# Performance work log

Measured on AMD Instinct MI355X. Metric: run time of the kernel, lower is better.

## Reference

```python
import jax, jax.numpy as jnp
import numpy as np
from jax import lax

C = 768
CA = C // 4  # adapter_channels = 192
L = 197      # 1 CLS + 14*14 patches
T_FRAMES = 16
B = 16
N = B * T_FRAMES


def quick_gelu(x):
    return x * jax.nn.sigmoid(1.702 * x)


def setup_inputs() -> dict:
    key = jax.random.key(0)
    ks = jax.random.split(key, 16)
    s = 0.02
    return {
        "x": jax.random.normal(ks[0], (L, N, C), dtype=jnp.float32),
        "T": T_FRAMES,
        # main path (fc1 -> depthwise conv1d over T -> fc2)
        "fc1_w": jax.random.normal(ks[1], (C, CA), jnp.float32) * s,
        "fc1_b": jnp.zeros((CA,), jnp.float32),
        "conv_w": jax.random.normal(ks[2], (CA, 1, 3), jnp.float32) * s,  # (O, I/g, K)
        "conv_b": jnp.zeros((CA,), jnp.float32),
        "fc2_w": jax.random.normal(ks[3], (CA, C), jnp.float32) * s,
        "fc2_b": jnp.zeros((C,), jnp.float32),
        # offset adapter (fc1 -> depthwise conv3d (1,3,3) -> fc2)
        "off_fc1_w": jax.random.normal(ks[4], (C, CA), jnp.float32) * s,
        "off_fc1_b": jnp.zeros((CA,), jnp.float32),
        "off_conv_w": jax.random.normal(ks[5], (CA, 1, 1, 3, 3), jnp.float32) * s,  # (O, I/g, D, H, W)
        "off_conv_b": jnp.zeros((CA,), jnp.float32),
        "off_fc2_w": jax.random.normal(ks[6], (CA, C), jnp.float32) * s,
        "off_fc2_b": jnp.zeros((C,), jnp.float32),
        # mlp branch (c_in -> QuickGELU -> c_out)
        "mlp_in_w": jax.random.normal(ks[7], (C, CA), jnp.float32) * s,
        "mlp_in_b": jnp.zeros((CA,), jnp.float32),
        "mlp_out_w": jax.random.normal(ks[8], (CA, C), jnp.float32) * s,
        "mlp_out_b": jnp.zeros((C,), jnp.float32),
    }


def _offset_adapter(x, T, fc1_w, fc1_b, conv_w, conv_b, fc2_w, fc2_b):
    Lx, Nx, Cx = x.shape
    Bx = Nx // T
    HW = Lx - 1
    H = int(round(HW ** 0.5))
    Ca = fc1_w.shape[1]
    xp = jnp.transpose(x, (1, 0, 2))            # (N, L, C)
    xs = xp[:, 1:, :].reshape(Bx, T, HW, Cx)    # (B, T, HW, C)
    # former frame: index [0, 0, 1, ..., T-2]
    x_former = jnp.concatenate([xs[:, :1], xs[:, :-1]], axis=1)
    off = xs - x_former
    off = off @ fc1_w + fc1_b                   # (B, T, HW, Ca)
    off = off.reshape(Bx, T, H, H, Ca).transpose(0, 4, 1, 2, 3)  # (B, Ca, T, H, W)
    off = lax.conv_general_dilated(
        off, conv_w, window_strides=(1, 1, 1),
        padding=[(0, 0), (1, 1), (1, 1)],
        dimension_numbers=("NCDHW", "OIDHW", "NCDHW"),
        feature_group_count=Ca,
    ) + conv_b[None, :, None, None, None]
    off = off.transpose(0, 2, 3, 4, 1).reshape(Nx, HW, Ca)
    off = off @ fc2_w + fc2_b                   # (N, L-1, C)
    return jnp.transpose(off, (1, 0, 2))        # (L-1, N, C)


def reference(x, T, fc1_w, fc1_b, conv_w, conv_b, fc2_w, fc2_b,
              off_fc1_w, off_fc1_b, off_conv_w, off_conv_b, off_fc2_w, off_fc2_b,
              mlp_in_w, mlp_in_b, mlp_out_w, mlp_out_b):
    Lx, Nx, Cx = x.shape
    Bx = Nx // T
    Ca = fc1_w.shape[1]

    offset = _offset_adapter(x, T, off_fc1_w, off_fc1_b, off_conv_w, off_conv_b,
                             off_fc2_w, off_fc2_b)  # (L-1, N, C)

    # mlp identity branch
    x_id = quick_gelu(x @ mlp_in_w + mlp_in_b) @ mlp_out_w + mlp_out_b  # (L, N, C)

    # main branch: fc1 -> depthwise conv1d along T -> fc2
    h = x @ fc1_w + fc1_b                                   # (L, N, Ca)
    h = jnp.transpose(h, (1, 0, 2)).reshape(Bx, T, Lx, Ca)  # (B, T, L, Ca)
    h = h.transpose(0, 2, 3, 1).reshape(Bx * Lx, Ca, T)     # (B*L, Ca, T)
    h = lax.conv_general_dilated(
        h, conv_w, window_strides=(1,), padding=[(1, 1)],
        dimension_numbers=("NCH", "OIH", "NCH"),
        feature_group_count=Ca,
    ) + conv_b[None, :, None]
    h = h.transpose(0, 2, 1).reshape(Bx, Lx, T, Ca)
    h = h.transpose(0, 2, 1, 3).reshape(Nx, Lx, Ca)
    h = jnp.transpose(h, (1, 0, 2))                         # (L, N, Ca)
    h = h @ fc2_w + fc2_b                                   # (L, N, C)

    x_id = x_id.at[1:].add(offset)
    return h + x_id
```

## Files before the change

kernel.cpp:

```cpp
#include <hip/hip_runtime.h>

#define L_DIM 197
#define N_DIM 256
#define C_DIM 768
#define CA_DIM 192
#define M_DIM (L_DIM * N_DIM)

typedef short s16x8 __attribute__((ext_vector_type(8)));
typedef float f32x4 __attribute__((ext_vector_type(4)));

__device__ __forceinline__ unsigned short f2bf(float f) {
  unsigned x = __builtin_bit_cast(unsigned, f);
  x = (x + 0x7fffu + ((x >> 16) & 1u)) >> 16;
  return (unsigned short)x;
}
__device__ __forceinline__ float bflo(unsigned u) { return __builtin_bit_cast(float, u << 16); }
__device__ __forceinline__ float bfhi(unsigned u) { return __builtin_bit_cast(float, u & 0xffff0000u); }

__device__ __forceinline__ void unp8(uint4 v, float* f) {
  f[0] = bflo(v.x); f[1] = bfhi(v.x); f[2] = bflo(v.y); f[3] = bfhi(v.y);
  f[4] = bflo(v.z); f[5] = bfhi(v.z); f[6] = bflo(v.w); f[7] = bfhi(v.w);
}

__device__ __forceinline__ void mfma16(f32x4& acc, s16x8 a, s16x8 b) {
  asm("v_mfma_f32_16x16x32_bf16 %0, %1, %2, %0" : "+v"(acc) : "v"(a), "v"(b));
}

typedef const void __attribute__((address_space(1)))* gp_t;
typedef void __attribute__((address_space(3)))* lp_t;
__device__ __forceinline__ void gl16(const void* g, void* l) {
  __builtin_amdgcn_global_load_lds((gp_t)g, (lp_t)l, 16, 0, 0);
}

#define WAITVM(n) asm volatile("s_waitcnt vmcnt(" #n ")" ::: "memory")

__device__ __forceinline__ int swz(int pid, int nwg) {
  const int q = nwg >> 3, r = nwg & 7, x = pid & 7, s = pid >> 3;
  return (x < r ? x * (q + 1) : r * (q + 1) + (x - r) * q) + s;
}

__global__ __launch_bounds__(256) void prep_k(
    const float* __restrict__ fc1_w, const float* __restrict__ mlp_in_w,
    const float* __restrict__ off_fc1_w, const float* __restrict__ fc2_w,
    const float* __restrict__ mlp_out_w, const float* __restrict__ off_fc2_w,
    unsigned short* __restrict__ wa, unsigned short* __restrict__ wc) {
  __shared__ float t[32][33];
  const int b = blockIdx.x;
  const int job = b / 144, tt = b - job * 144;
  const float* in = job == 0 ? fc1_w : job == 1 ? mlp_in_w : job == 2 ? off_fc1_w
                  : job == 3 ? fc2_w : job == 4 ? mlp_out_w : off_fc2_w;
  const int Cc = job < 3 ? 192 : 768;
  const int tc = Cc >> 5;
  const int tr0 = (tt / tc) << 5, tc0 = (tt - (tt / tc) * tc) << 5;
  const int lr = threadIdx.x >> 5, lc = threadIdx.x & 31;
#pragma unroll
  for (int p = 0; p < 4; p++)
    t[p * 8 + lr][lc] = in[(tr0 + p * 8 + lr) * Cc + tc0 + lc];
  __syncthreads();
#pragma unroll
  for (int p = 0; p < 4; p++) {
    const int orow = tc0 + p * 8 + lr;
    const int ocol = tr0 + lc;
    const unsigned short v = f2bf(t[lc][p * 8 + lr]);
    if (job < 3) wa[(job * 192 + orow) * 768 + ocol] = v;
    else         wc[orow * 576 + (job - 3) * 192 + ocol] = v;
  }
}

__global__ __launch_bounds__(256) void xcvt_k(const float* __restrict__ x,
                                              unsigned short* __restrict__ xb) {
  const int total8 = M_DIM * C_DIM / 8;
  const int step = gridDim.x * 256;
  for (int i = blockIdx.x * 256 + threadIdx.x; i < total8; i += step) {
    const float4 a = *(const float4*)(x + (size_t)i * 8);
    const float4 b = *(const float4*)(x + (size_t)i * 8 + 4);
    s16x8 v;
    v[0] = (short)f2bf(a.x); v[1] = (short)f2bf(a.y);
    v[2] = (short)f2bf(a.z); v[3] = (short)f2bf(a.w);
    v[4] = (short)f2bf(b.x); v[5] = (short)f2bf(b.y);
    v[6] = (short)f2bf(b.z); v[7] = (short)f2bf(b.w);
    *(s16x8*)(xb + (size_t)i * 8) = v;
  }
}

__global__ __launch_bounds__(256, 2) void gemm_a_k(
    const unsigned short* __restrict__ xb, const unsigned short* __restrict__ wa,
    const float* __restrict__ fc1_b, const float* __restrict__ mlp_in_b,
    const float* __restrict__ cw, const float* __restrict__ cb,
    const float* __restrict__ off_b1, unsigned short* __restrict__ hcat) {
  __shared__ unsigned short As[2][64 * 32];
  __shared__ unsigned short Bs[2][576 * 32];
  const int tid = threadIdx.x, lane = tid & 63, w = tid >> 6;
  const int m0 = blockIdx.x * 64;

  const int sr = tid >> 2, sc = (tid & 3) * 8;
  const unsigned short* gA = xb + (size_t)(m0 + sr) * C_DIM + sc;
  const unsigned short* gB = wa + (size_t)sr * C_DIM + sc;

  auto stage = [&](int kt, int b) {
    gl16(gA + kt * 32, &As[b][sr * 32 + sc]);
    const unsigned short* pb = gB + kt * 32;
#pragma unroll
    for (int j = 0; j < 9; j++)
      gl16(pb + (size_t)j * 64 * C_DIM, &Bs[b][(j * 64 + sr) * 32 + sc]);
  };

  f32x4 acc[4][9];
#pragma unroll
  for (int i = 0; i < 4; i++)
#pragma unroll
    for (int j = 0; j < 9; j++) acc[i][j] = (f32x4){0.f, 0.f, 0.f, 0.f};

  const int fr = lane & 15, fq = lane >> 4;
  const int wn = w * 144;

  stage(0, 0);
  __syncthreads();
#pragma unroll 2
  for (int kt = 0; kt < 24; ++kt) {
    const int b = kt & 1;
    if (kt + 1 < 24) stage(kt + 1, b ^ 1);
    s16x8 af[4];
#pragma unroll
    for (int mi = 0; mi < 4; mi++)
      af[mi] = *(const s16x8*)&As[b][(mi * 16 + fr) * 32 + fq * 8];
#pragma unroll
    for (int ni = 0; ni < 9; ni++) {
      const s16x8 bf_ = *(const s16x8*)&Bs[b][(wn + ni * 16 + fr) * 32 + fq * 8];
#pragma unroll
      for (int mi = 0; mi < 4; mi++) mfma16(acc[mi][ni], af[mi], bf_);
    }
    __syncthreads();
  }

  const bool zrow = (m0 < 256);
#pragma unroll
  for (int ni = 0; ni < 9; ni++) {
    const int cb_ = wn + ni * 16;
    const int path = cb_ / 192;
    const int ca = cb_ % 192 + fr;
    if (path == 0) {
      const float bv = fc1_b[ca];
      const float w0 = cw[ca * 3], w1 = cw[ca * 3 + 1], w2 = cw[ca * 3 + 2];
      const float cbv = cb[ca];
#pragma unroll
      for (int mi = 0; mi < 4; mi++) {
        const float v0 = acc[mi][ni][0] + bv, v1 = acc[mi][ni][1] + bv;
        const float v2 = acc[mi][ni][2] + bv, v3 = acc[mi][ni][3] + bv;
        const float pv3 = __shfl_up(v3, 16);
        const float nv0 = __shfl_down(v0, 16);
        const float p0 = fq > 0 ? pv3 : 0.f;
        const float n3 = fq < 3 ? nv0 : 0.f;
        const int mb = m0 + mi * 16 + fq * 4;
        hcat[(size_t)(mb + 0) * 576 + ca] = f2bf(w0 * p0 + w1 * v0 + w2 * v1 + cbv);
        hcat[(size_t)(mb + 1) * 576 + ca] = f2bf(w0 * v0 + w1 * v1 + w2 * v2 + cbv);
        hcat[(size_t)(mb + 2) * 576 + ca] = f2bf(w0 * v1 + w1 * v2 + w2 * v3 + cbv);
        hcat[(size_t)(mb + 3) * 576 + ca] = f2bf(w0 * v2 + w1 * v3 + w2 * n3 + cbv);
      }
    } else if (path == 1) {
      const float bv = mlp_in_b[ca];
#pragma unroll
      for (int mi = 0; mi < 4; mi++)
#pragma unroll
        for (int r = 0; r < 4; r++) {
          const int m = m0 + mi * 16 + fq * 4 + r;
          float v = acc[mi][ni][r] + bv;
          v = v / (1.f + __expf(-1.702f * v));
          hcat[(size_t)m * 576 + 192 + ca] = f2bf(v);
        }
    } else {
      const float bv = off_b1[ca];
#pragma unroll
      for (int mi = 0; mi < 4; mi++) {
        const float v0 = acc[mi][ni][0], v1 = acc[mi][ni][1];
        const float v2 = acc[mi][ni][2], v3 = acc[mi][ni][3];
        const float pv3 = __shfl_up(v3, 16);
        const int mb = m0 + mi * 16 + fq * 4;
        const float o0 = (fq == 0) ? bv : (v0 - pv3 + bv);
        if (zrow) {
          hcat[(size_t)(mb + 0) * 576 + 384 + ca] = 0;
          hcat[(size_t)(mb + 1) * 576 + 384 + ca] = 0;
          hcat[(size_t)(mb + 2) * 576 + 384 + ca] = 0;
          hcat[(size_t)(mb + 3) * 576 + 384 + ca] = 0;
        } else {
          hcat[(size_t)(mb + 0) * 576 + 384 + ca] = f2bf(o0);
          hcat[(size_t)(mb + 1) * 576 + 384 + ca] = f2bf(v1 - v0 + bv);
          hcat[(size_t)(mb + 2) * 576 + 384 + ca] = f2bf(v2 - v1 + bv);
          hcat[(size_t)(mb + 3) * 576 + 384 + ca] = f2bf(v3 - v2 + bv);
        }
      }
    }
  }
}

__global__ __launch_bounds__(256) void conv3d_k(
    const float* __restrict__ w3, const float* __restrict__ b2,
    unsigned short* __restrict__ hcat) {
  __shared__ float ds[196 * 48];
  __shared__ float w3s[9 * 48];
  __shared__ float b2s[48];
  const int blk = blockIdx.x;
  const int n = blk >> 2, q = blk & 3;
  const int ch0 = q * 48;
  const int tid = threadIdx.x;

  for (int j = tid; j < 432; j += 256) {
    const int c = j / 9, tap = j % 9;
    w3s[tap * 48 + c] = w3[(ch0 + c) * 9 + tap];
  }
  if (tid < 48) b2s[tid] = b2[ch0 + tid];

  for (int j = tid; j < 196 * 6; j += 256) {
    const int hw = j / 6, ck = j % 6;
    float dv[8];
    unp8(*(const uint4*)(hcat + ((size_t)(1 + hw) * 256 + n) * 576 + 384 + ch0 + ck * 8), dv);
#pragma unroll
    for (int e = 0; e < 8; e++) ds[hw * 48 + ck * 8 + e] = dv[e];
  }
  __syncthreads();

  for (int j = tid; j < 196 * 6; j += 256) {
    const int hw = j / 6, ck = j % 6;
    const int i = hw / 14, j0 = hw - i * 14;
    float acc[8];
#pragma unroll
    for (int e = 0; e < 8; e++) acc[e] = b2s[ck * 8 + e];
#pragma unroll
    for (int di = 0; di < 3; di++) {
      const int ii = i + di - 1;
      if (ii < 0 || ii >= 14) continue;
#pragma unroll
      for (int dj = 0; dj < 3; dj++) {
        const int jc = j0 + dj - 1;
        if (jc < 0 || jc >= 14) continue;
        const float* dp = &ds[(ii * 14 + jc) * 48 + ck * 8];
        const float* wp = &w3s[(di * 3 + dj) * 48 + ck * 8];
#pragma unroll
        for (int e = 0; e < 8; e++) acc[e] += wp[e] * dp[e];
      }
    }
    unsigned o[4];
#pragma unroll
    for (int e = 0; e < 8; e += 2)
      o[e / 2] = (unsigned)f2bf(acc[e]) | ((unsigned)f2bf(acc[e + 1]) << 16);
    uint4 ov; ov.x = o[0]; ov.y = o[1]; ov.z = o[2]; ov.w = o[3];
    *(uint4*)(hcat + ((size_t)(1 + hw) * 256 + n) * 576 + 384 + ch0 + ck * 8) = ov;
  }
}

__global__ __launch_bounds__(256, 1) void gemm_c_k(
    const unsigned short* __restrict__ hcat, const unsigned short* __restrict__ wc,
    const float* __restrict__ fc2_b, const float* __restrict__ mlp_out_b,
    const float* __restrict__ off_fc2_b, float* __restrict__ out) {
  __shared__ unsigned short As[3][128 * 32];
  __shared__ unsigned short Bs[3][256 * 32];
  const int tid = threadIdx.x, lane = tid & 63, w = tid >> 6;
  const int lid = swz(blockIdx.x, 3 * 394);
  const int by = lid / 3, bx = lid - by * 3;
  const int m0 = by * 128, n0 = bx * 256;

  const int sr = tid >> 2, sc = (tid & 3) * 8;
  const unsigned short* gA = hcat + (size_t)(m0 + sr) * 576 + sc;
  const unsigned short* gB = wc + (size_t)(n0 + sr) * 576 + sc;
  auto stage = [&](int kt, int b) {
#pragma unroll
    for (int j = 0; j < 2; j++)
      gl16(gA + kt * 32 + j * 64 * 576, &As[b][(sr + j * 64) * 32 + sc]);
#pragma unroll
    for (int j = 0; j < 4; j++)
      gl16(gB + kt * 32 + j * 64 * 576, &Bs[b][(sr + j * 64) * 32 + sc]);
  };

  f32x4 acc[4][8];
#pragma unroll
  for (int i = 0; i < 4; i++)
#pragma unroll
    for (int j = 0; j < 8; j++) acc[i][j] = (f32x4){0.f, 0.f, 0.f, 0.f};

  const int fr = lane & 15, fq = lane >> 4;
  const int wm = (w >> 1) * 64, wn = (w & 1) * 128;

  stage(0, 0);
#pragma unroll 3
  for (int kt = 0; kt < 18; ++kt) {
    const int b = kt % 3;
    if (kt + 1 < 18) { stage(kt + 1, (kt + 1) % 3); WAITVM(6); }
    else             { WAITVM(0); }
    __builtin_amdgcn_s_barrier();
    asm volatile("" ::: "memory");
    s16x8 af[4], bfv[8];
#pragma unroll
    for (int mi = 0; mi < 4; mi++)
      af[mi] = *(const s16x8*)&As[b][(wm + mi * 16 + fr) * 32 + fq * 8];
#pragma unroll
    for (int ni = 0; ni < 8; ni++)
      bfv[ni] = *(const s16x8*)&Bs[b][(wn + ni * 16 + fr) * 32 + fq * 8];
#pragma unroll
    for (int mi = 0; mi < 4; mi++)
#pragma unroll
      for (int ni = 0; ni < 8; ni++) mfma16(acc[mi][ni], af[mi], bfv[ni]);
  }

  float bv[8];
#pragma unroll
  for (int ni = 0; ni < 8; ni++) {
    const int c = n0 + wn + ni * 16 + fr;
    bv[ni] = fc2_b[c] + mlp_out_b[c] + (by >= 2 ? off_fc2_b[c] : 0.f);
  }
#pragma unroll
  for (int mi = 0; mi < 4; mi++)
#pragma unroll
    for (int r = 0; r < 4; r++) {
      const int m = m0 + wm + mi * 16 + fq * 4 + r;
      float* op = out + (size_t)m * C_DIM + n0 + wn;
#pragma unroll
      for (int ni = 0; ni < 8; ni++) op[ni * 16 + fr] = acc[mi][ni][r] + bv[ni];
    }
}

extern "C" void kernel_launch(void* const* d_in, const int* in_sizes, int n_in,
                              void* d_out, int out_size, void* d_ws, size_t ws_size,
                              hipStream_t stream) {
  const float* x          = (const float*)d_in[0];
  const float* fc1_w      = (const float*)d_in[2];
  const float* fc1_b      = (const float*)d_in[3];
  const float* conv_w     = (const float*)d_in[4];
  const float* conv_b     = (const float*)d_in[5];
  const float* fc2_w      = (const float*)d_in[6];
  const float* fc2_b      = (const float*)d_in[7];
  const float* off_fc1_w  = (const float*)d_in[8];
  const float* off_fc1_b  = (const float*)d_in[9];
  const float* off_conv_w = (const float*)d_in[10];
  const float* off_conv_b = (const float*)d_in[11];
  const float* off_fc2_w  = (const float*)d_in[12];
  const float* off_fc2_b  = (const float*)d_in[13];
  const float* mlp_in_w   = (const float*)d_in[14];
  const float* mlp_in_b   = (const float*)d_in[15];
  const float* mlp_out_w  = (const float*)d_in[16];
  const float* mlp_out_b  = (const float*)d_in[17];
  float* out = (float*)d_out;

  char* ws = (char*)d_ws;
  unsigned short* xb   = (unsigned short*)(ws);
  unsigned short* hcat = (unsigned short*)(ws + (size_t)M_DIM * C_DIM * 2);
  unsigned short* wa   = (unsigned short*)(ws + (size_t)M_DIM * C_DIM * 2
                                              + (size_t)M_DIM * 576 * 2);
  unsigned short* wc   = wa + (size_t)576 * 768;

  prep_k<<<864, 256, 0, stream>>>(fc1_w, mlp_in_w, off_fc1_w, fc2_w, mlp_out_w,
                                  off_fc2_w, wa, wc);
  xcvt_k<<<2048, 256, 0, stream>>>(x, xb);
  gemm_a_k<<<788, 256, 0, stream>>>(xb, wa, fc1_b, mlp_in_b, conv_w, conv_b,
                                    off_fc1_b, hcat);
  conv3d_k<<<1024, 256, 0, stream>>>(off_conv_w, off_conv_b, hcat);
  gemm_c_k<<<1182, 256, 0, stream>>>(hcat, wc, fc2_b, mlp_out_b, off_fc2_b, out);
}
```

Baseline: 228.8 us.

## Retile first GEMM to 128x288 with triple-buffered loads and fuse prep kernels

The first GEMM now uses 128-row by 288-column tiles, with two blocks per row band instead of one 64x576 block. Each wave covers a 64x144 sub-tile, and blocks are ordered by a swizzled mapping so weight tiles see better L2 reuse. The shared-memory pipeline goes from two to three buffers, using manual vmcnt waits and a single barrier per k-step instead of two __syncthreads. The weight transpose and x-to-bf16 conversion kernels are merged into one launch to save a kernel launch. The hand-written vmcnt counts depend on how many loads each wave issues, so any miscount risks a race.

New measurement: 209.8 us. 8.3% less time.

```diff
diff --git a/kernel.cpp b/kernel.cpp
--- a/kernel.cpp
+++ b/kernel.cpp
@@ -39,47 +39,48 @@
   return (x < r ? x * (q + 1) : r * (q + 1) + (x - r) * q) + s;
 }
 
-__global__ __launch_bounds__(256) void prep_k(
+__global__ __launch_bounds__(256) void prep_xcvt_k(
     const float* __restrict__ fc1_w, const float* __restrict__ mlp_in_w,
     const float* __restrict__ off_fc1_w, const float* __restrict__ fc2_w,
     const float* __restrict__ mlp_out_w, const float* __restrict__ off_fc2_w,
-    unsigned short* __restrict__ wa, unsigned short* __restrict__ wc) {
+    const float* __restrict__ x,
+    unsigned short* __restrict__ wa, unsigned short* __restrict__ wc,
+    unsigned short* __restrict__ xb) {
   __shared__ float t[32][33];
   const int b = blockIdx.x;
-  const int job = b / 144, tt = b - job * 144;
-  const float* in = job == 0 ? fc1_w : job == 1 ? mlp_in_w : job == 2 ? off_fc1_w
-                  : job == 3 ? fc2_w : job == 4 ? mlp_out_w : off_fc2_w;
-  const int Cc = job < 3 ? 192 : 768;
-  const int tc = Cc >> 5;
-  const int tr0 = (tt / tc) << 5, tc0 = (tt - (tt / tc) * tc) << 5;
-  const int lr = threadIdx.x >> 5, lc = threadIdx.x & 31;
-#pragma unroll
-  for (int p = 0; p < 4; p++)
-    t[p * 8 + lr][lc] = in[(tr0 + p * 8 + lr) * Cc + tc0 + lc];
-  __syncthreads();
-#pragma unroll
-  for (int p = 0; p < 4; p++) {
-    const int orow = tc0 + p * 8 + lr;
-    const int ocol = tr0 + lc;
-    const unsigned short v = f2bf(t[lc][p * 8 + lr]);
-    if (job < 3) wa[(job * 192 + orow) * 768 + ocol] = v;
-    else         wc[orow * 576 + (job - 3) * 192 + ocol] = v;
-  }
-}
-
-__global__ __launch_bounds__(256) void xcvt_k(const float* __restrict__ x,
-                                              unsigned short* __restrict__ xb) {
-  const int total8 = M_DIM * C_DIM / 8;
-  const int step = gridDim.x * 256;
-  for (int i = blockIdx.x * 256 + threadIdx.x; i < total8; i += step) {
-    const float4 a = *(const float4*)(x + (size_t)i * 8);
-    const float4 b = *(const float4*)(x + (size_t)i * 8 + 4);
-    s16x8 v;
-    v[0] = (short)f2bf(a.x); v[1] = (short)f2bf(a.y);
-    v[2] = (short)f2bf(a.z); v[3] = (short)f2bf(a.w);
-    v[4] = (short)f2bf(b.x); v[5] = (short)f2bf(b.y);
-    v[6] = (short)f2bf(b.z); v[7] = (short)f2bf(b.w);
-    *(s16x8*)(xb + (size_t)i * 8) = v;
+  if (b < 864) {
+    const int job = b / 144, tt = b - job * 144;
+    const float* in = job == 0 ? fc1_w : job == 1 ? mlp_in_w : job == 2 ? off_fc1_w
+                    : job == 3 ? fc2_w : job == 4 ? mlp_out_w : off_fc2_w;
+    const int Cc = job < 3 ? 192 : 768;
+    const int tc = Cc >> 5;
+    const int tr0 = (tt / tc) << 5, tc0 = (tt - (tt / tc) * tc) << 5;
+    const int lr = threadIdx.x >> 5, lc = threadIdx.x & 31;
+#pragma unroll
+    for (int p = 0; p < 4; p++)
+      t[p * 8 + lr][lc] = in[(tr0 + p * 8 + lr) * Cc + tc0 + lc];
+    __syncthreads();
+#pragma unroll
+    for (int p = 0; p < 4; p++) {
+      const int orow = tc0 + p * 8 + lr;
+      const int ocol = tr0 + lc;
+      const unsigned short v = f2bf(t[lc][p * 8 + lr]);
+      if (job < 3) wa[(job * 192 + orow) * 768 + ocol] = v;
+      else         wc[orow * 576 + (job - 3) * 192 + ocol] = v;
+    }
+  } else {
+    const int total8 = M_DIM * C_DIM / 8;
+    const int step = 2048 * 256;
+    for (int i = (b - 864) * 256 + threadIdx.x; i < total8; i += step) {
+      const float4 a = *(const float4*)(x + (size_t)i * 8);
+      const float4 c = *(const float4*)(x + (size_t)i * 8 + 4);
+      s16x8 v;
+      v[0] = (short)f2bf(a.x); v[1] = (short)f2bf(a.y);
+      v[2] = (short)f2bf(a.z); v[3] = (short)f2bf(a.w);
+      v[4] = (short)f2bf(c.x); v[5] = (short)f2bf(c.y);
+      v[6] = (short)f2bf(c.z); v[7] = (short)f2bf(c.w);
+      *(s16x8*)(xb + (size_t)i * 8) = v;
+    }
   }
 }
 
@@ -88,21 +89,27 @@
     const float* __restrict__ fc1_b, const float* __restrict__ mlp_in_b,
     const float* __restrict__ cw, const float* __restrict__ cb,
     const float* __restrict__ off_b1, unsigned short* __restrict__ hcat) {
-  __shared__ unsigned short As[2][64 * 32];
-  __shared__ unsigned short Bs[2][576 * 32];
+  __shared__ unsigned short As[3][128 * 32];
+  __shared__ unsigned short Bs[3][288 * 32];
   const int tid = threadIdx.x, lane = tid & 63, w = tid >> 6;
-  const int m0 = blockIdx.x * 64;
+  const int lid = swz(blockIdx.x, 2 * 394);
+  const int by = lid >> 1, bx = lid & 1;
+  const int m0 = by * 128, n0 = bx * 288;
 
   const int sr = tid >> 2, sc = (tid & 3) * 8;
   const unsigned short* gA = xb + (size_t)(m0 + sr) * C_DIM + sc;
-  const unsigned short* gB = wa + (size_t)sr * C_DIM + sc;
+  const unsigned short* gB = wa + (size_t)(n0 + sr) * C_DIM + sc;
 
   auto stage = [&](int kt, int b) {
-    gl16(gA + kt * 32, &As[b][sr * 32 + sc]);
+    const unsigned short* pa = gA + kt * 32;
+    gl16(pa,              &As[b][sr * 32 + sc]);
+    gl16(pa + 64 * C_DIM, &As[b][(64 + sr) * 32 + sc]);
     const unsigned short* pb = gB + kt * 32;
 #pragma unroll
-    for (int j = 0; j < 9; j++)
+    for (int j = 0; j < 4; j++)
       gl16(pb + (size_t)j * 64 * C_DIM, &Bs[b][(j * 64 + sr) * 32 + sc]);
+    if (tid < 128)
+      gl16(pb + (size_t)256 * C_DIM, &Bs[b][(256 + sr) * 32 + sc]);
   };
 
   f32x4 acc[4][9];
@@ -112,33 +119,38 @@
     for (int j = 0; j < 9; j++) acc[i][j] = (f32x4){0.f, 0.f, 0.f, 0.f};
 
   const int fr = lane & 15, fq = lane >> 4;
-  const int wn = w * 144;
+  const int wm = (w >> 1) * 64, wn = (w & 1) * 144;
 
   stage(0, 0);
-  __syncthreads();
-#pragma unroll 2
+#pragma unroll 3
   for (int kt = 0; kt < 24; ++kt) {
-    const int b = kt & 1;
-    if (kt + 1 < 24) stage(kt + 1, b ^ 1);
+    const int b = kt % 3;
+    if (kt + 1 < 24) {
+      stage(kt + 1, (kt + 1) % 3);
+      if (w < 2) { WAITVM(7); } else { WAITVM(6); }
+    } else {
+      WAITVM(0);
+    }
+    __builtin_amdgcn_s_barrier();
+    asm volatile("" ::: "memory");
     s16x8 af[4];
 #pragma unroll
     for (int mi = 0; mi < 4; mi++)
-      af[mi] = *(const s16x8*)&As[b][(mi * 16 + fr) * 32 + fq * 8];
+      af[mi] = *(const s16x8*)&As[b][(wm + mi * 16 + fr) * 32 + fq * 8];
 #pragma unroll
     for (int ni = 0; ni < 9; ni++) {
       const s16x8 bf_ = *(const s16x8*)&Bs[b][(wn + ni * 16 + fr) * 32 + fq * 8];
 #pragma unroll
       for (int mi = 0; mi < 4; mi++) mfma16(acc[mi][ni], af[mi], bf_);
     }
-    __syncthreads();
-  }
-
-  const bool zrow = (m0 < 256);
+  }
+
+  const bool zrow = (by < 2);
 #pragma unroll
   for (int ni = 0; ni < 9; ni++) {
-    const int cb_ = wn + ni * 16;
+    const int cb_ = n0 + wn + ni * 16;
     const int path = cb_ / 192;
-    const int ca = cb_ % 192 + fr;
+    const int ca = cb_ - path * 192 + fr;
     if (path == 0) {
       const float bv = fc1_b[ca];
       const float w0 = cw[ca * 3], w1 = cw[ca * 3 + 1], w2 = cw[ca * 3 + 2];
@@ -151,7 +163,7 @@
         const float nv0 = __shfl_down(v0, 16);
         const float p0 = fq > 0 ? pv3 : 0.f;
         const float n3 = fq < 3 ? nv0 : 0.f;
-        const int mb = m0 + mi * 16 + fq * 4;
+        const int mb = m0 + wm + mi * 16 + fq * 4;
         hcat[(size_t)(mb + 0) * 576 + ca] = f2bf(w0 * p0 + w1 * v0 + w2 * v1 + cbv);
         hcat[(size_t)(mb + 1) * 576 + ca] = f2bf(w0 * v0 + w1 * v1 + w2 * v2 + cbv);
         hcat[(size_t)(mb + 2) * 576 + ca] = f2bf(w0 * v1 + w1 * v2 + w2 * v3 + cbv);
@@ -163,7 +175,7 @@
       for (int mi = 0; mi < 4; mi++)
 #pragma unroll
         for (int r = 0; r < 4; r++) {
-          const int m = m0 + mi * 16 + fq * 4 + r;
+          const int m = m0 + wm + mi * 16 + fq * 4 + r;
           float v = acc[mi][ni][r] + bv;
           v = v / (1.f + __expf(-1.702f * v));
           hcat[(size_t)m * 576 + 192 + ca] = f2bf(v);
@@ -175,7 +187,7 @@
         const float v0 = acc[mi][ni][0], v1 = acc[mi][ni][1];
         const float v2 = acc[mi][ni][2], v3 = acc[mi][ni][3];
         const float pv3 = __shfl_up(v3, 16);
-        const int mb = m0 + mi * 16 + fq * 4;
+        const int mb = m0 + wm + mi * 16 + fq * 4;
         const float o0 = (fq == 0) ? bv : (v0 - pv3 + bv);
         if (zrow) {
           hcat[(size_t)(mb + 0) * 576 + 384 + ca] = 0;
@@ -347,9 +359,8 @@
                                               + (size_t)M_DIM * 576 * 2);
   unsigned short* wc   = wa + (size_t)576 * 768;
 
-  prep_k<<<864, 256, 0, stream>>>(fc1_w, mlp_in_w, off_fc1_w, fc2_w, mlp_out_w,
-                                  off_fc2_w, wa, wc);
-  xcvt_k<<<2048, 256, 0, stream>>>(x, xb);
+  prep_xcvt_k<<<2912, 256, 0, stream>>>(fc1_w, mlp_in_w, off_fc1_w, fc2_w,
+                                        mlp_out_w, off_fc2_w, x, wa, wc, xb);
   gemm_a_k<<<788, 256, 0, stream>>>(xb, wa, fc1_b, mlp_in_b, conv_w, conv_b,
                                     off_fc1_b, hcat);
   conv3d_k<<<1024, 256, 0, stream>>>(off_conv_w, off_conv_b, hcat);
```
